# Kernel tuning notes

Hardware: AMD Instinct MI355X
Metric: run time of the kernel (lower is better)

The kernel has to match this reference:

```python
import jax, jax.numpy as jnp
import numpy as np

N_NODES = 100000
N_EDGES = 1600000


def gcn_conv(x, W, b, src, dst, n):
    # PyG GCNConv: x @ W, add self-loops, symmetric deg^{-1/2} normalization,
    # sum-aggregate messages from src into dst, then add bias.
    h = x @ W  # [N, out]
    loops = jnp.arange(n, dtype=src.dtype)
    s = jnp.concatenate([src, loops])
    d = jnp.concatenate([dst, loops])
    deg = jax.ops.segment_sum(jnp.ones_like(d, dtype=h.dtype), d, num_segments=n)
    dinv = 1.0 / jnp.sqrt(deg)  # deg >= 1 thanks to self-loops
    norm = dinv[s] * dinv[d]  # [E + N]
    msg = h[s] * norm[:, None]
    out = jax.ops.segment_sum(msg, d, num_segments=n)
    return out + b


def setup_inputs() -> dict:
    key = jax.random.key(0)
    k1, k2, k3, k4 = jax.random.split(key, 4)
    x = jax.random.normal(k1, (N_NODES, 64), dtype=jnp.float32)
    edge_index = jax.random.randint(k2, (2, N_EDGES), 0, N_NODES, dtype=jnp.int64)
    W1 = jax.random.normal(k3, (64, 32), dtype=jnp.float32) * (1.0 / np.sqrt(64))
    b1 = jnp.zeros((32,), dtype=jnp.float32)
    W2 = jax.random.normal(k4, (32, 16), dtype=jnp.float32) * (1.0 / np.sqrt(32))
    b2 = jnp.zeros((16,), dtype=jnp.float32)
    return {"x": x, "edge_index": edge_index, "W1": W1, "b1": b1, "W2": W2, "b2": b2}


def reference(x, edge_index, W1, b1, W2, b2):
    n = x.shape[0]
    src, dst = edge_index[0], edge_index[1]
    h = gcn_conv(x, W1, b1, src, dst, n)
    h = jax.nn.relu(h)
    h = gcn_conv(h, W2, b2, src, dst, n)
    return jax.nn.log_softmax(h, axis=1)
```

## Files before the change

kernel.cpp:

```cpp
#include <hip/hip_runtime.h>
#include <hip/hip_bf16.h>


#define FEAT_IN 64
#define FEAT_H  32
#define FEAT_O  16
#define MAXNB   512
#define PART_G  512
#define MAXSNB  256
#define SPART   8192

__device__ __forceinline__ float2 upk_bf2(unsigned w) {
    return make_float2(__uint_as_float(w << 16), __uint_as_float(w & 0xFFFF0000u));
}

__device__ __forceinline__ int wave_incl_scan(int x, int lane) {
#pragma unroll
    for (int off = 1; off < 64; off <<= 1) {
        int y = __shfl_up(x, off);
        if (lane >= off) x += y;
    }
    return x;
}

__global__ void k_hist(const int* __restrict__ dst, int e,
                       int* __restrict__ hist, int G, int NBk) {
    __shared__ int lh[MAXNB];
    int t = threadIdx.x, g = blockIdx.x;
    for (int i = t; i < NBk; i += 256) lh[i] = 0;
    __syncthreads();
    int chunk = (((e + G - 1) / G) + 3) & ~3;
    int beg = g * chunk, end = min(e, beg + chunk);
    if ((e & 3) == 0) {
        int vend = beg + ((end - beg) & ~3);
        for (int j = beg + 4 * t; j + 3 < vend; j += 1024) {
            int4 d = *(const int4*)&dst[j];
            atomicAdd(&lh[d.x >> 8], 1);
            atomicAdd(&lh[d.y >> 8], 1);
            atomicAdd(&lh[d.z >> 8], 1);
            atomicAdd(&lh[d.w >> 8], 1);
        }
        for (int j = vend + t; j < end; j += 256) atomicAdd(&lh[dst[j] >> 8], 1);
    } else {
        for (int i = beg + t; i < end; i += 256) atomicAdd(&lh[dst[i] >> 8], 1);
    }
    __syncthreads();
    for (int i = t; i < NBk; i += 256) hist[(size_t)i * G + g] = lh[i];
}

__global__ void k_scan1(const int* __restrict__ in, int* __restrict__ out,
                        int* __restrict__ bsum, int len) {
    __shared__ int wsum[4];
    int t = threadIdx.x;
    int base = blockIdx.x * 1024 + t * 4;
    int a0 = (base + 0) < len ? in[base + 0] : 0;
    int a1 = (base + 1) < len ? in[base + 1] : 0;
    int a2 = (base + 2) < len ? in[base + 2] : 0;
    int a3 = (base + 3) < len ? in[base + 3] : 0;
    int tsum = a0 + a1 + a2 + a3;
    int lane = t & 63, wid = t >> 6;
    int x = wave_incl_scan(tsum, lane);
    if (lane == 63) wsum[wid] = x;
    __syncthreads();
    int woff = 0;
#pragma unroll
    for (int w = 0; w < 4; ++w) woff += (w < wid) ? wsum[w] : 0;
    int ex = x + woff - tsum;
    if (base + 0 < len) out[base + 0] = ex;
    if (base + 1 < len) out[base + 1] = ex + a0;
    if (base + 2 < len) out[base + 2] = ex + a0 + a1;
    if (base + 3 < len) out[base + 3] = ex + a0 + a1 + a2;
    if (t == 255) bsum[blockIdx.x] = x + woff;
}

__device__ __forceinline__ void scan_bsum(const int* __restrict__ bsum, int snb,
                                          int* __restrict__ sps, int t) {
    __shared__ int wsb[4];
    int v = (t < snb) ? bsum[t] : 0;
    int lane = t & 63, wid = t >> 6;
    int x = wave_incl_scan(v, lane);
    if (lane == 63) wsb[wid] = x;
    __syncthreads();
    int woff = 0;
#pragma unroll
    for (int w = 0; w < 4; ++w) woff += (w < wid) ? wsb[w] : 0;
    sps[t] = x + woff - v;
    __syncthreads();
}

__global__ void k_partition(const int* __restrict__ src, const int* __restrict__ dst, int e,
                            const int* __restrict__ base, const int* __restrict__ bsum,
                            int snb, int* __restrict__ part, int G, int NBk) {
    __shared__ int cur[MAXNB];
    __shared__ int sps[MAXSNB];
    int t = threadIdx.x, g = blockIdx.x;
    scan_bsum(bsum, snb, sps, t);
    for (int i = t; i < NBk; i += 256) {
        size_t idx = (size_t)i * G + g;
        cur[i] = base[idx] + sps[idx >> 10];
    }
    __syncthreads();
    int chunk = (((e + G - 1) / G) + 3) & ~3;
    int beg = g * chunk, end = min(e, beg + chunk);
    if ((e & 3) == 0) {
        int vend = beg + ((end - beg) & ~3);
        for (int j = beg + 4 * t; j + 3 < vend; j += 1024) {
            int4 s4 = *(const int4*)&src[j];
            int4 d4 = *(const int4*)&dst[j];
            int p0 = atomicAdd(&cur[d4.x >> 8], 1); part[p0] = s4.x | ((d4.x & 255) << 24);
            int p1 = atomicAdd(&cur[d4.y >> 8], 1); part[p1] = s4.y | ((d4.y & 255) << 24);
            int p2 = atomicAdd(&cur[d4.z >> 8], 1); part[p2] = s4.z | ((d4.z & 255) << 24);
            int p3 = atomicAdd(&cur[d4.w >> 8], 1); part[p3] = s4.w | ((d4.w & 255) << 24);
        }
        for (int j = vend + t; j < end; j += 256) {
            int s_ = src[j], d_ = dst[j];
            int pos = atomicAdd(&cur[d_ >> 8], 1);
            part[pos] = s_ | ((d_ & 255) << 24);
        }
    } else {
        for (int i = beg + t; i < end; i += 256) {
            int s_ = src[i], d_ = dst[i];
            int pos = atomicAdd(&cur[d_ >> 8], 1);
            part[pos] = s_ | ((d_ & 255) << 24);
        }
    }
}

__global__ void k_bucket_csr(const int* __restrict__ part, const int* __restrict__ base,
                             const int* __restrict__ bsum, int snb, int e, int G, int NBk,
                             int n, int* __restrict__ row_start, int* __restrict__ col,
                             float* __restrict__ dinv) {
    __shared__ int cntq[256][4];
    __shared__ int curq[256][4];
    __shared__ int spre[256];
    __shared__ int sps[MAXSNB];
    __shared__ int wsc[4];
    __shared__ int spart[SPART];
    int t = threadIdx.x, b = blockIdx.x;
    scan_bsum(bsum, snb, sps, t);
    size_t ib = (size_t)b * G;
    size_t ie = (size_t)(b + 1) * G;
    int beg = base[ib] + sps[ib >> 10];
    int end = (b == NBk - 1) ? e : (base[ie] + sps[ie >> 10]);
    int m = end - beg;
    int qt = (n + 3) >> 2;
    int q1 = qt, q2 = 2 * qt, q3 = 3 * qt;
#pragma unroll
    for (int q = 0; q < 4; ++q) { cntq[t][q] = 0; curq[t][q] = 0; }
    __syncthreads();
    bool fits = (m <= SPART);
    if (fits) {
        for (int j = t; j < m; j += 256) {
            int r = part[beg + j];
            spart[j] = r;
            int s = r & 0x00FFFFFF;
            int q = (s >= q1) + (s >= q2) + (s >= q3);
            atomicAdd(&cntq[((unsigned)r) >> 24][q], 1);
        }
    } else {
        for (int j = t; j < m; j += 256) {
            int r = part[beg + j];
            int s = r & 0x00FFFFFF;
            int q = (s >= q1) + (s >= q2) + (s >= q3);
            atomicAdd(&cntq[((unsigned)r) >> 24][q], 1);
        }
    }
    __syncthreads();
    int c0 = cntq[t][0], c1 = cntq[t][1], c2 = cntq[t][2], c3 = cntq[t][3];
    int v = c0 + c1 + c2 + c3;
    int lane = t & 63, wid = t >> 6;
    int x = wave_incl_scan(v, lane);
    if (lane == 63) wsc[wid] = x;
    cntq[t][0] = 0; cntq[t][1] = c0; cntq[t][2] = c0 + c1; cntq[t][3] = c0 + c1 + c2;
    __syncthreads();
    int woff = 0;
#pragma unroll
    for (int w = 0; w < 4; ++w) woff += (w < wid) ? wsc[w] : 0;
    int pre = x + woff - v;
    spre[t] = pre;
    int node = b * 256 + t;
    if (node < n) {
        row_start[node] = beg + pre;
        dinv[node] = rsqrtf((float)v + 1.0f);
    }
    if (b == NBk - 1 && t == 0) row_start[n] = e;
    __syncthreads();
    if (fits) {
        for (int j = t; j < m; j += 256) {
            int r = spart[j];
            int dl = ((unsigned)r) >> 24;
            int s = r & 0x00FFFFFF;
            int q = (s >= q1) + (s >= q2) + (s >= q3);
            int off = atomicAdd(&curq[dl][q], 1);
            col[beg + spre[dl] + cntq[dl][q] + off] = s;
        }
    } else {
        for (int j = t; j < m; j += 256) {
            int r = part[beg + j];
            int dl = ((unsigned)r) >> 24;
            int s = r & 0x00FFFFFF;
            int q = (s >= q1) + (s >= q2) + (s >= q3);
            int off = atomicAdd(&curq[dl][q], 1);
            col[beg + spre[dl] + cntq[dl][q] + off] = s;
        }
    }
}

__global__ void k_gemm1(const float* __restrict__ x, const float* __restrict__ W1,
                        const float* __restrict__ dinv,
                        __hip_bfloat162* __restrict__ h1s2, int n) {
    __shared__ float sW[FEAT_IN * FEAT_H];
    __shared__ float sx[16][FEAT_IN + 1];
    int t = threadIdx.x;
    for (int i = t; i < FEAT_IN * FEAT_H; i += 256) sW[i] = W1[i];
#pragma unroll
    for (int tile = 0; tile < 2; ++tile) {
        int nodeBase = blockIdx.x * 32 + tile * 16;
        __syncthreads();
        {
            int xn = t >> 4, c = t & 15;
            int node = nodeBase + xn;
            if (node < n) {
                float4 v = ((const float4*)x)[(size_t)node * 16 + c];
                sx[xn][c * 4 + 0] = v.x; sx[xn][c * 4 + 1] = v.y;
                sx[xn][c * 4 + 2] = v.z; sx[xn][c * 4 + 3] = v.w;
            }
        }
        __syncthreads();
        int nl = t >> 4, g = t & 15;
        int node = nodeBase + nl;
        if (node < n) {
            float a0 = 0.0f, a1 = 0.0f;
#pragma unroll
            for (int k = 0; k < FEAT_IN; ++k) {
                float s = sx[nl][k];
                a0 += s * sW[k * FEAT_H + 2 * g];
                a1 += s * sW[k * FEAT_H + 2 * g + 1];
            }
            float dv = dinv[node];
            __hip_bfloat162 o;
            o.x = __float2bfloat16(a0 * dv);
            o.y = __float2bfloat16(a1 * dv);
            h1s2[(size_t)node * 16 + g] = o;
        }
    }
}

#define ACC8(u) do { float2 p_;                         \
    p_ = upk_bf2((u).x); a[0] += p_.x; a[1] += p_.y;    \
    p_ = upk_bf2((u).y); a[2] += p_.x; a[3] += p_.y;    \
    p_ = upk_bf2((u).z); a[4] += p_.x; a[5] += p_.y;    \
    p_ = upk_bf2((u).w); a[6] += p_.x; a[7] += p_.y; } while (0)

__global__ void k_gather1_gemm2(const int* __restrict__ row_start, const int* __restrict__ col,
                                const uint4* __restrict__ h1q, const float* __restrict__ W2,
                                const float* __restrict__ b1,
                                const float* __restrict__ dinv,
                                __hip_bfloat162* __restrict__ h2s2, int n) {
    __shared__ float sW[FEAT_H * FEAT_O];
    __shared__ float sb1[FEAT_H];
    __shared__ float sz[64][FEAT_H + 1];
    int t = threadIdx.x;
    for (int i = t; i < FEAT_H * FEAT_O; i += 256) sW[i] = W2[i];
    if (t < FEAT_H) sb1[t] = b1[t];
    __syncthreads();

    int g = t >> 2, l = t & 3;
    int d = blockIdx.x * 64 + g;
    if (d < n) {
        float a[8];
        {
            uint4 u = h1q[(size_t)d * 4 + l];
            float2 p;
            p = upk_bf2(u.x); a[0] = p.x; a[1] = p.y;
            p = upk_bf2(u.y); a[2] = p.x; a[3] = p.y;
            p = upk_bf2(u.z); a[4] = p.x; a[5] = p.y;
            p = upk_bf2(u.w); a[6] = p.x; a[7] = p.y;
        }
        int beg = row_start[d], end = row_start[d + 1];
        int j = beg;
        for (; j + 8 <= end; j += 8) {
            int c0 = col[j + 0], c1 = col[j + 1], c2 = col[j + 2], c3 = col[j + 3];
            int c4 = col[j + 4], c5 = col[j + 5], c6 = col[j + 6], c7 = col[j + 7];
            uint4 u0 = h1q[(size_t)c0 * 4 + l];
            uint4 u1 = h1q[(size_t)c1 * 4 + l];
            uint4 u2 = h1q[(size_t)c2 * 4 + l];
            uint4 u3 = h1q[(size_t)c3 * 4 + l];
            uint4 u4 = h1q[(size_t)c4 * 4 + l];
            uint4 u5 = h1q[(size_t)c5 * 4 + l];
            uint4 u6 = h1q[(size_t)c6 * 4 + l];
            uint4 u7 = h1q[(size_t)c7 * 4 + l];
            ACC8(u0); ACC8(u1); ACC8(u2); ACC8(u3);
            ACC8(u4); ACC8(u5); ACC8(u6); ACC8(u7);
        }
        for (; j + 4 <= end; j += 4) {
            int c0 = col[j + 0], c1 = col[j + 1], c2 = col[j + 2], c3 = col[j + 3];
            uint4 u0 = h1q[(size_t)c0 * 4 + l];
            uint4 u1 = h1q[(size_t)c1 * 4 + l];
            uint4 u2 = h1q[(size_t)c2 * 4 + l];
            uint4 u3 = h1q[(size_t)c3 * 4 + l];
            ACC8(u0); ACC8(u1); ACC8(u2); ACC8(u3);
        }
        for (; j < end; ++j) {
            uint4 u = h1q[(size_t)col[j] * 4 + l];
            ACC8(u);
        }
        float dv = dinv[d];
#pragma unroll
        for (int k = 0; k < 8; ++k)
            sz[g][l * 8 + k] = fmaxf(dv * a[k] + sb1[l * 8 + k], 0.0f);
    }
    __syncthreads();
#pragma unroll
    for (int it = 0; it < 2; ++it) {
        int nl = (t >> 3) + it * 32;
        int m = t & 7;
        int node = blockIdx.x * 64 + nl;
        if (node < n) {
            float a0 = 0.0f, a1 = 0.0f;
#pragma unroll
            for (int f = 0; f < FEAT_H; ++f) {
                float z = sz[nl][f];
                a0 += z * sW[f * FEAT_O + 2 * m];
                a1 += z * sW[f * FEAT_O + 2 * m + 1];
            }
            float dv = dinv[node];
            __hip_bfloat162 o;
            o.x = __float2bfloat16(a0 * dv);
            o.y = __float2bfloat16(a1 * dv);
            h2s2[(size_t)node * 8 + m] = o;
        }
    }
}

__global__ void k_gather2_lsm(const int* __restrict__ row_start, const int* __restrict__ col,
                              const uint4* __restrict__ h2q, const float* __restrict__ b2,
                              const float* __restrict__ dinv,
                              float4* __restrict__ out4, int n) {
    __shared__ float sb2[FEAT_O];
    int t = threadIdx.x;
    if (t < FEAT_O) sb2[t] = b2[t];
    __syncthreads();
    int g = t >> 1, h = t & 1;
    int d = blockIdx.x * 128 + g;
    if (d >= n) return;
    float a[8];
    {
        uint4 u = h2q[(size_t)d * 2 + h];
        float2 p;
        p = upk_bf2(u.x); a[0] = p.x; a[1] = p.y;
        p = upk_bf2(u.y); a[2] = p.x; a[3] = p.y;
        p = upk_bf2(u.z); a[4] = p.x; a[5] = p.y;
        p = upk_bf2(u.w); a[6] = p.x; a[7] = p.y;
    }
    int beg = row_start[d], end = row_start[d + 1];
    int j = beg;
    for (; j + 8 <= end; j += 8) {
        int c0 = col[j + 0], c1 = col[j + 1], c2 = col[j + 2], c3 = col[j + 3];
        int c4 = col[j + 4], c5 = col[j + 5], c6 = col[j + 6], c7 = col[j + 7];
        uint4 u0 = h2q[(size_t)c0 * 2 + h];
        uint4 u1 = h2q[(size_t)c1 * 2 + h];
        uint4 u2 = h2q[(size_t)c2 * 2 + h];
        uint4 u3 = h2q[(size_t)c3 * 2 + h];
        uint4 u4 = h2q[(size_t)c4 * 2 + h];
        uint4 u5 = h2q[(size_t)c5 * 2 + h];
        uint4 u6 = h2q[(size_t)c6 * 2 + h];
        uint4 u7 = h2q[(size_t)c7 * 2 + h];
        ACC8(u0); ACC8(u1); ACC8(u2); ACC8(u3);
        ACC8(u4); ACC8(u5); ACC8(u6); ACC8(u7);
    }
    for (; j + 4 <= end; j += 4) {
        int c0 = col[j + 0], c1 = col[j + 1], c2 = col[j + 2], c3 = col[j + 3];
        uint4 u0 = h2q[(size_t)c0 * 2 + h];
        uint4 u1 = h2q[(size_t)c1 * 2 + h];
        uint4 u2 = h2q[(size_t)c2 * 2 + h];
        uint4 u3 = h2q[(size_t)c3 * 2 + h];
        ACC8(u0); ACC8(u1); ACC8(u2); ACC8(u3);
    }
    for (; j < end; ++j) {
        uint4 u = h2q[(size_t)col[j] * 2 + h];
        ACC8(u);
    }
    float dv = dinv[d];
    float v[8];
    float mx = -1e30f;
#pragma unroll
    for (int k = 0; k < 8; ++k) {
        v[k] = dv * a[k] + sb2[h * 8 + k];
        mx = fmaxf(mx, v[k]);
    }
    mx = fmaxf(mx, __shfl_xor(mx, 1));
    float ssum = 0.0f;
#pragma unroll
    for (int k = 0; k < 8; ++k) ssum += __expf(v[k] - mx);
    ssum += __shfl_xor(ssum, 1);
    float lg = mx + logf(ssum);
    float4 o0 = { v[0] - lg, v[1] - lg, v[2] - lg, v[3] - lg };
    float4 o1 = { v[4] - lg, v[5] - lg, v[6] - lg, v[7] - lg };
    out4[(size_t)d * 4 + h * 2 + 0] = o0;
    out4[(size_t)d * 4 + h * 2 + 1] = o1;
}

extern "C" void kernel_launch(void* const* d_in, const int* in_sizes, int n_in,
                              void* d_out, int out_size, void* d_ws, size_t ws_size,
                              hipStream_t stream) {
    const float* x  = (const float*)d_in[0];
    const int*   ei = (const int*)d_in[1];
    const float* W1 = (const float*)d_in[2];
    const float* b1 = (const float*)d_in[3];
    const float* W2 = (const float*)d_in[4];
    const float* b2 = (const float*)d_in[5];

    const int n = in_sizes[0] / FEAT_IN;
    const int e = in_sizes[1] / 2;
    const int* src = ei;
    const int* dst = ei + e;
    const int NBk = (n + 255) >> 8;
    const int G = PART_G;
    const int hlen = NBk * G;
    const int snb = (hlen + 1023) / 1024;

    int* part = (int*)d_ws;
    __hip_bfloat162* h1s2 = (__hip_bfloat162*)d_ws;
    int* col  = (int*)d_ws + e;
    __hip_bfloat162* h2s2 = (__hip_bfloat162*)(col + e);
    float* dinv = (float*)(h2s2 + 8 * (size_t)n);
    int* hist      = (int*)(dinv + n);
    int* base      = hist + hlen;
    int* bsum      = base + hlen;
    int* row_start = bsum + MAXSNB;

    k_hist<<<G, 256, 0, stream>>>(dst, e, hist, G, NBk);
    k_scan1<<<snb, 256, 0, stream>>>(hist, base, bsum, hlen);
    k_partition<<<G, 256, 0, stream>>>(src, dst, e, base, bsum, snb, part, G, NBk);
    k_bucket_csr<<<NBk, 256, 0, stream>>>(part, base, bsum, snb, e, G, NBk, n,
                                          row_start, col, dinv);

    k_gemm1<<<(n + 31) / 32, 256, 0, stream>>>(x, W1, dinv, h1s2, n);
    k_gather1_gemm2<<<(n + 63) / 64, 256, 0, stream>>>(row_start, col, (const uint4*)h1s2,
                                                       W2, b1, dinv, h2s2, n);
    k_gather2_lsm<<<(n + 127) / 128, 256, 0, stream>>>(row_start, col, (const uint4*)h2s2,
                                                       b2, dinv, (float4*)d_out, n);
}
```

Baseline: 179.5 us.

## Split layer-1 features into two halves and gather each in a separate pass

The 32-wide bf16 hidden features are stored as two separate 16-feature arrays. The first aggregation kernel now walks each node's neighbor list twice, once per half, with 2 lanes per node and 128 nodes per block instead of 4 lanes and 64 nodes. Each pass gathers from a table half the size, which is meant to improve cache hit rates for the random neighbor reads. The cost is reading the column indices twice and doing more serial work per thread. The gather loop is also moved into a shared macro.

```diff
diff --git a/kernel.cpp b/kernel.cpp
--- a/kernel.cpp
+++ b/kernel.cpp
@@ -208,7 +208,8 @@
 
 __global__ void k_gemm1(const float* __restrict__ x, const float* __restrict__ W1,
                         const float* __restrict__ dinv,
-                        __hip_bfloat162* __restrict__ h1s2, int n) {
+                        __hip_bfloat162* __restrict__ h1a2,
+                        __hip_bfloat162* __restrict__ h1b2, int n) {
     __shared__ float sW[FEAT_IN * FEAT_H];
     __shared__ float sx[16][FEAT_IN + 1];
     int t = threadIdx.x;
@@ -241,7 +242,8 @@
             __hip_bfloat162 o;
             o.x = __float2bfloat16(a0 * dv);
             o.y = __float2bfloat16(a1 * dv);
-            h1s2[(size_t)node * 16 + g] = o;
+            if (g < 8) h1a2[(size_t)node * 8 + g] = o;
+            else       h1b2[(size_t)node * 8 + (g - 8)] = o;
         }
     }
 }
@@ -252,70 +254,87 @@
     p_ = upk_bf2((u).z); a[4] += p_.x; a[5] += p_.y;    \
     p_ = upk_bf2((u).w); a[6] += p_.x; a[7] += p_.y; } while (0)
 
+#define GATHER_PASS(hq) do {                                        \
+    int j = beg;                                                    \
+    for (; j + 8 <= end; j += 8) {                                  \
+        int c0 = col[j + 0], c1 = col[j + 1], c2 = col[j + 2], c3 = col[j + 3]; \
+        int c4 = col[j + 4], c5 = col[j + 5], c6 = col[j + 6], c7 = col[j + 7]; \
+        uint4 u0 = (hq)[(size_t)c0 * 2 + h];                        \
+        uint4 u1 = (hq)[(size_t)c1 * 2 + h];                        \
+        uint4 u2 = (hq)[(size_t)c2 * 2 + h];                        \
+        uint4 u3 = (hq)[(size_t)c3 * 2 + h];                        \
+        uint4 u4 = (hq)[(size_t)c4 * 2 + h];                        \
+        uint4 u5 = (hq)[(size_t)c5 * 2 + h];                        \
+        uint4 u6 = (hq)[(size_t)c6 * 2 + h];                        \
+        uint4 u7 = (hq)[(size_t)c7 * 2 + h];                        \
+        ACC8(u0); ACC8(u1); ACC8(u2); ACC8(u3);                     \
+        ACC8(u4); ACC8(u5); ACC8(u6); ACC8(u7);                     \
+    }                                                               \
+    for (; j + 4 <= end; j += 4) {                                  \
+        int c0 = col[j + 0], c1 = col[j + 1], c2 = col[j + 2], c3 = col[j + 3]; \
+        uint4 u0 = (hq)[(size_t)c0 * 2 + h];                        \
+        uint4 u1 = (hq)[(size_t)c1 * 2 + h];                        \
+        uint4 u2 = (hq)[(size_t)c2 * 2 + h];                        \
+        uint4 u3 = (hq)[(size_t)c3 * 2 + h];                        \
+        ACC8(u0); ACC8(u1); ACC8(u2); ACC8(u3);                     \
+    }                                                               \
+    for (; j < end; ++j) {                                          \
+        uint4 u = (hq)[(size_t)col[j] * 2 + h];                     \
+        ACC8(u);                                                    \
+    }                                                               \
+} while (0)
+
 __global__ void k_gather1_gemm2(const int* __restrict__ row_start, const int* __restrict__ col,
-                                const uint4* __restrict__ h1q, const float* __restrict__ W2,
+                                const uint4* __restrict__ h1aq, const uint4* __restrict__ h1bq,
+                                const float* __restrict__ W2,
                                 const float* __restrict__ b1,
                                 const float* __restrict__ dinv,
                                 __hip_bfloat162* __restrict__ h2s2, int n) {
     __shared__ float sW[FEAT_H * FEAT_O];
     __shared__ float sb1[FEAT_H];
-    __shared__ float sz[64][FEAT_H + 1];
+    __shared__ float sz[128][FEAT_H + 1];
     int t = threadIdx.x;
     for (int i = t; i < FEAT_H * FEAT_O; i += 256) sW[i] = W2[i];
     if (t < FEAT_H) sb1[t] = b1[t];
     __syncthreads();
 
-    int g = t >> 2, l = t & 3;
-    int d = blockIdx.x * 64 + g;
+    int g = t >> 1, h = t & 1;
+    int d = blockIdx.x * 128 + g;
     if (d < n) {
+        int beg = row_start[d], end = row_start[d + 1];
+        float dv = dinv[d];
         float a[8];
         {
-            uint4 u = h1q[(size_t)d * 4 + l];
+            uint4 u = h1aq[(size_t)d * 2 + h];
             float2 p;
             p = upk_bf2(u.x); a[0] = p.x; a[1] = p.y;
             p = upk_bf2(u.y); a[2] = p.x; a[3] = p.y;
             p = upk_bf2(u.z); a[4] = p.x; a[5] = p.y;
             p = upk_bf2(u.w); a[6] = p.x; a[7] = p.y;
         }
-        int beg = row_start[d], end = row_start[d + 1];
-        int j = beg;
-        for (; j + 8 <= end; j += 8) {
-            int c0 = col[j + 0], c1 = col[j + 1], c2 = col[j + 2], c3 = col[j + 3];
-            int c4 = col[j + 4], c5 = col[j + 5], c6 = col[j + 6], c7 = col[j + 7];
-            uint4 u0 = h1q[(size_t)c0 * 4 + l];
-            uint4 u1 = h1q[(size_t)c1 * 4 + l];
-            uint4 u2 = h1q[(size_t)c2 * 4 + l];
-            uint4 u3 = h1q[(size_t)c3 * 4 + l];
-            uint4 u4 = h1q[(size_t)c4 * 4 + l];
-            uint4 u5 = h1q[(size_t)c5 * 4 + l];
-            uint4 u6 = h1q[(size_t)c6 * 4 + l];
-            uint4 u7 = h1q[(size_t)c7 * 4 + l];
-            ACC8(u0); ACC8(u1); ACC8(u2); ACC8(u3);
-            ACC8(u4); ACC8(u5); ACC8(u6); ACC8(u7);
-        }
-        for (; j + 4 <= end; j += 4) {
-            int c0 = col[j + 0], c1 = col[j + 1], c2 = col[j + 2], c3 = col[j + 3];
-            uint4 u0 = h1q[(size_t)c0 * 4 + l];
-            uint4 u1 = h1q[(size_t)c1 * 4 + l];
-            uint4 u2 = h1q[(size_t)c2 * 4 + l];
-            uint4 u3 = h1q[(size_t)c3 * 4 + l];
-            ACC8(u0); ACC8(u1); ACC8(u2); ACC8(u3);
-        }
-        for (; j < end; ++j) {
-            uint4 u = h1q[(size_t)col[j] * 4 + l];
-            ACC8(u);
-        }
-        float dv = dinv[d];
+        GATHER_PASS(h1aq);
 #pragma unroll
         for (int k = 0; k < 8; ++k)
-            sz[g][l * 8 + k] = fmaxf(dv * a[k] + sb1[l * 8 + k], 0.0f);
-    }
-    __syncthreads();
-#pragma unroll
-    for (int it = 0; it < 2; ++it) {
+            sz[g][h * 8 + k] = fmaxf(dv * a[k] + sb1[h * 8 + k], 0.0f);
+        {
+            uint4 u = h1bq[(size_t)d * 2 + h];
+            float2 p;
+            p = upk_bf2(u.x); a[0] = p.x; a[1] = p.y;
+            p = upk_bf2(u.y); a[2] = p.x; a[3] = p.y;
+            p = upk_bf2(u.z); a[4] = p.x; a[5] = p.y;
+            p = upk_bf2(u.w); a[6] = p.x; a[7] = p.y;
+        }
+        GATHER_PASS(h1bq);
+#pragma unroll
+        for (int k = 0; k < 8; ++k)
+            sz[g][16 + h * 8 + k] = fmaxf(dv * a[k] + sb1[16 + h * 8 + k], 0.0f);
+    }
+    __syncthreads();
+#pragma unroll
+    for (int it = 0; it < 4; ++it) {
         int nl = (t >> 3) + it * 32;
         int m = t & 7;
-        int node = blockIdx.x * 64 + nl;
+        int node = blockIdx.x * 128 + nl;
         if (node < n) {
             float a0 = 0.0f, a1 = 0.0f;
 #pragma unroll
@@ -354,33 +373,7 @@
         p = upk_bf2(u.w); a[6] = p.x; a[7] = p.y;
     }
     int beg = row_start[d], end = row_start[d + 1];
-    int j = beg;
-    for (; j + 8 <= end; j += 8) {
-        int c0 = col[j + 0], c1 = col[j + 1], c2 = col[j + 2], c3 = col[j + 3];
-        int c4 = col[j + 4], c5 = col[j + 5], c6 = col[j + 6], c7 = col[j + 7];
-        uint4 u0 = h2q[(size_t)c0 * 2 + h];
-        uint4 u1 = h2q[(size_t)c1 * 2 + h];
-        uint4 u2 = h2q[(size_t)c2 * 2 + h];
-        uint4 u3 = h2q[(size_t)c3 * 2 + h];
-        uint4 u4 = h2q[(size_t)c4 * 2 + h];
-        uint4 u5 = h2q[(size_t)c5 * 2 + h];
-        uint4 u6 = h2q[(size_t)c6 * 2 + h];
-        uint4 u7 = h2q[(size_t)c7 * 2 + h];
-        ACC8(u0); ACC8(u1); ACC8(u2); ACC8(u3);
-        ACC8(u4); ACC8(u5); ACC8(u6); ACC8(u7);
-    }
-    for (; j + 4 <= end; j += 4) {
-        int c0 = col[j + 0], c1 = col[j + 1], c2 = col[j + 2], c3 = col[j + 3];
-        uint4 u0 = h2q[(size_t)c0 * 2 + h];
-        uint4 u1 = h2q[(size_t)c1 * 2 + h];
-        uint4 u2 = h2q[(size_t)c2 * 2 + h];
-        uint4 u3 = h2q[(size_t)c3 * 2 + h];
-        ACC8(u0); ACC8(u1); ACC8(u2); ACC8(u3);
-    }
-    for (; j < end; ++j) {
-        uint4 u = h2q[(size_t)col[j] * 2 + h];
-        ACC8(u);
-    }
+    GATHER_PASS(h2q);
     float dv = dinv[d];
     float v[8];
     float mx = -1e30f;
@@ -421,7 +414,8 @@
     const int snb = (hlen + 1023) / 1024;
 
     int* part = (int*)d_ws;
-    __hip_bfloat162* h1s2 = (__hip_bfloat162*)d_ws;
+    __hip_bfloat162* h1a2 = (__hip_bfloat162*)d_ws;
+    __hip_bfloat162* h1b2 = h1a2 + 8 * (size_t)n;
     int* col  = (int*)d_ws + e;
     __hip_bfloat162* h2s2 = (__hip_bfloat162*)(col + e);
     float* dinv = (float*)(h2s2 + 8 * (size_t)n);
@@ -436,9 +430,11 @@
     k_bucket_csr<<<NBk, 256, 0, stream>>>(part, base, bsum, snb, e, G, NBk, n,
                                           row_start, col, dinv);
 
-    k_gemm1<<<(n + 31) / 32, 256, 0, stream>>>(x, W1, dinv, h1s2, n);
-    k_gather1_gemm2<<<(n + 63) / 64, 256, 0, stream>>>(row_start, col, (const uint4*)h1s2,
-                                                       W2, b1, dinv, h2s2, n);
+    k_gemm1<<<(n + 31) / 32, 256, 0, stream>>>(x, W1, dinv, h1a2, h1b2, n);
+    k_gather1_gemm2<<<(n + 127) / 128, 256, 0, stream>>>(row_start, col,
+                                                         (const uint4*)h1a2,
+                                                         (const uint4*)h1b2,
+                                                         W2, b1, dinv, h2s2, n);
     k_gather2_lsm<<<(n + 127) / 128, 256, 0, stream>>>(row_start, col, (const uint4*)h2s2,
                                                        b2, dinv, (float4*)d_out, n);
 }
```

Measured after the change: 186.5 us. +3.9%, slower.
